# Kernel tuning notes

Hardware: AMD Instinct MI355X
Metric: run time of the kernel (lower is better)

## Reference

```python
import jax, jax.numpy as jnp
import numpy as np

MANTISA_BIT = 8.0  # mantisa_bit init arg


def conv3d(x, w, b, stride=1, pad=1):
    # x: [N,C,D,H,W], w: [O,I,kD,kH,kW]
    out = jax.lax.conv_general_dilated(
        x, w,
        window_strides=(stride, stride, stride),
        padding=[(pad, pad)] * 3,
        dimension_numbers=("NCDHW", "OIDHW", "NCDHW"),
    )
    return out + b.reshape(1, -1, 1, 1, 1)


def bfp_quant(x, ch_exp, m_bits):
    # Block floating point: shared per-channel exponent ch_exp [C],
    # signed mantissa with m_bits total bits. scale = 2^(m-1-exp);
    # q = clip(round(x*scale), -(2^(m-1)-1), 2^(m-1)-1)/scale
    scale = jnp.exp2(m_bits - 1.0 - ch_exp).reshape(1, -1, 1, 1, 1)
    lim = 2.0 ** (m_bits - 1.0) - 1.0
    return jnp.clip(jnp.round(x * scale), -lim, lim) / scale


def setup_inputs() -> dict:
    key = jax.random.key(0)
    ks = jax.random.split(key, 7)
    N, C_in, C_out, T, H, W, K = 8, 64, 64, 16, 56, 56, 3
    x = jax.random.normal(ks[0], (N, C_in, T, H, W), jnp.float32)
    w1 = jax.random.normal(ks[1], (C_out, C_in, K, K, K), jnp.float32) * 0.05
    b1 = jax.random.normal(ks[2], (C_out,), jnp.float32) * 0.05
    w2 = jax.random.normal(ks[3], (C_out, C_out, K, K, K), jnp.float32) * 0.05
    b2 = jax.random.normal(ks[4], (C_out,), jnp.float32) * 0.05
    # offline-optimized per-channel shared exponents (opt_exp_act_list[0], [1])
    exp1 = jax.random.randint(ks[5], (C_out,), 2, 6).astype(jnp.float32)
    exp2 = jax.random.randint(ks[6], (C_out,), 2, 6).astype(jnp.float32)
    return {"x": x, "w1": w1, "b1": b1, "w2": w2, "b2": b2,
            "exp1": exp1, "exp2": exp2}


def reference(x, w1, b1, w2, b2, exp1, exp2):
    # conv1 -> BFP quant -> ReLU
    res = conv3d(x, w1, b1)
    res = jax.nn.relu(bfp_quant(res, exp1, MANTISA_BIT))
    # conv2 -> BFP quant
    res = conv3d(res, w2, b2)
    res = bfp_quant(res, exp2, MANTISA_BIT)
    # identity shortcut (downsample=False) quantized with opt_exp_act_list[1]
    x_q = bfp_quant(x, exp2, MANTISA_BIT)
    return jax.nn.relu(x_q + res)
```

## Files before the change

kernel.cpp:

```cpp
#include <hip/hip_runtime.h>
#include <hip/hip_bf16.h>

#define Nn 8
#define Cc 64
#define Tt 16
#define Hh 56
#define Ww 56

typedef __bf16 bf16x8 __attribute__((ext_vector_type(8)));
typedef float f32x16 __attribute__((ext_vector_type(16)));
typedef unsigned short u16;
typedef unsigned int u32;

__device__ __forceinline__ u16 f32_to_bf16(float f) {
    u32 u = __float_as_uint(f);
    u32 r = (u + 0x7FFFu + ((u >> 16) & 1u)) >> 16;
    return (u16)r;
}
__device__ __forceinline__ float bf16_to_f32(u16 h) {
    return __uint_as_float(((u32)h) << 16);
}

__device__ __forceinline__ void gload16(const void* gsrc, void* lds) {
    __builtin_amdgcn_global_load_lds(
        (const __attribute__((address_space(1))) u32*)gsrc,
        (__attribute__((address_space(3))) u32*)lds, 16, 0, 0);
}

__global__ __launch_bounds__(256) void prep_w_kernel(
    const float* __restrict__ w1, const float* __restrict__ w2,
    u16* __restrict__ w1h, u16* __restrict__ w1l,
    u16* __restrict__ w2h, u16* __restrict__ w2l,
    u16* __restrict__ zpage)
{
    int idx = blockIdx.x * 256 + threadIdx.x;
    if (idx >= 221184) {
        ((uint4*)zpage)[idx - 221184] = make_uint4(0, 0, 0, 0);
        return;
    }
    int conv = idx / 110592;
    int rem  = idx % 110592;
    int tap  = rem >> 12;
    int co   = (rem >> 6) & 63;
    int ci   = rem & 63;
    const float* w = conv ? w2 : w1;
    float v = w[co * 1728 + ci * 27 + tap];
    u16 hi = f32_to_bf16(v);
    u16 lo = f32_to_bf16(v - bf16_to_f32(hi));
    int dst = tap * 4096 + co * 64 + ci;
    if (conv) { w2h[dst] = hi; w2l[dst] = lo; }
    else      { w1h[dst] = hi; w1l[dst] = lo; }
}

__global__ __launch_bounds__(256) void split_x_kernel(
    const float* __restrict__ x, u16* __restrict__ xh)
{
    __shared__ float tile[Cc][Hh + 1];
    const int tid = threadIdx.x;
    const int bid = blockIdx.x;
    const int h = bid % Hh;
    const int t = (bid / Hh) % Tt;
    const int n = bid / (Hh * Tt);
    for (int it = 0; it < 14; ++it) {
        int id = it * 256 + tid;
        int ci = id / Ww, w = id % Ww;
        tile[ci][w] = x[(((size_t)(n * Cc + ci) * Tt + t) * Hh + h) * Ww + w];
    }
    __syncthreads();
    const size_t obase = (size_t)bid * (Ww * Cc);
    for (int it = 0; it < 7; ++it) {
        int j = it * 256 + tid;
        int w = j >> 5, ci0 = (j & 31) << 1;
        u16 h0 = f32_to_bf16(tile[ci0][w]);
        u16 h1 = f32_to_bf16(tile[ci0 + 1][w]);
        *(ushort2*)(xh + obase + (size_t)w * Cc + ci0) = make_ushort2(h0, h1);
    }
}

#define SLICE_B 3712
#define A1_BUF  40960
#define B1_BUF  36864
#define C1_SMEM (2 * A1_BUF + 2 * B1_BUF)
#define C2_BOFF 40960
#define C2_SMEM 81920

__device__ __forceinline__ const bf16x8* frag_ptr(const char* base, int row, int slot) {
    int col = (slot * 16) ^ (((row >> 1) & 3) << 4);
    return (const bf16x8*)(base + row * 64 + col);
}

__global__ __launch_bounds__(512, 1) void conv1_mfma_kernel(
    const u16* __restrict__ xh,
    const u16* __restrict__ w1h, const u16* __restrict__ w1l,
    const float* __restrict__ b1, const float* __restrict__ e1,
    const u16* __restrict__ zpage, u16* __restrict__ res1)
{
    __shared__ __align__(16) char smem[C1_SMEM];

    const int tid = threadIdx.x;
    const int l = tid & 63, wid = tid >> 6;
    const int l31 = l & 31, hi5 = l >> 5;
    const int wbase = tid & ~63;
    const int bid = (blockIdx.x & 7) * 112 + (blockIdx.x >> 3);
    const int hb = bid % 7;
    const int t  = (bid / 7) % Tt;
    const int n  = bid / (7 * Tt);
    const int h0 = hb * 8;

    f32x16 acc[2][2] = {};

    auto ISSUE_A = [&](int slab, int abuf) {
        char* dst = smem + abuf * A1_BUF;
        const int cih = slab / 3, kd = slab % 3;
        const int td = t + kd - 1;
        const bool tdv = (td >= 0 && td < Tt);
        const size_t tdbase = (size_t)(n * Tt + (tdv ? td : 0)) * ((size_t)Hh * Ww * Cc);
#pragma unroll
        for (int it = 0; it < 5; ++it) {
            int fi = it * 512 + tid;
            int u = fi / 232, c = fi - u * 232;
            int r = c >> 2, slot = c & 3;
            int hh = h0 - 1 + u;
            int slog = slot ^ ((r >> 1) & 3);
            const u16* src = xh + tdbase
                + ((size_t)hh * Ww + (r - 1)) * Cc + cih * 32 + slog * 8;
            bool valid = tdv & (fi < 2320) & (hh >= 0) & (hh < Hh) & (r >= 1) & (r <= Ww);
            if (!valid) src = zpage;
            gload16(src, dst + (it * 512 + wbase) * 16);
        }
    };
    auto ISSUE_B = [&](int sub, int bbuf) {
        char* dst = smem + 2 * A1_BUF + bbuf * B1_BUF;
        const int slab = sub >> 1, hl = sub & 1;
        const int cih = slab / 3, kd = slab % 3;
        const u16* wsrc = hl ? w1l : w1h;
#pragma unroll
        for (int it = 0; it < 5; ++it) {
            int fi = it * 512 + tid;
            if (fi < 2304) {
                int u = fi >> 8, c = fi & 255;
                int co = c >> 2, slot = c & 3;
                int slog = slot ^ ((co >> 1) & 3);
                const u16* src = wsrc + (kd * 9 + u) * 4096 + co * 64 + cih * 32 + slog * 8;
                gload16(src, dst + (it * 512 + wbase) * 16);
            }
        }
    };

    ISSUE_A(0, 0);
    ISSUE_B(0, 0);
    asm volatile("s_waitcnt vmcnt(0)" ::: "memory");
    __builtin_amdgcn_s_barrier();
    __builtin_amdgcn_sched_barrier(0);

#pragma unroll 1
    for (int j = 0; j < 12; ++j) {
        if (j < 11) ISSUE_B(j + 1, (j + 1) & 1);
        if ((j & 1) && (j < 11)) ISSUE_A((j + 1) >> 1, ((j + 1) >> 1) & 1);
        __builtin_amdgcn_sched_barrier(0);
        const char* Acur = smem + (((j >> 1) & 1) * A1_BUF);
        const char* Bcur = smem + 2 * A1_BUF + ((j & 1) * B1_BUF);
        const char* Aw = Acur + (size_t)wid * SLICE_B;
#pragma unroll
        for (int kh = 0; kh < 3; ++kh) {
            const char* Ak = Aw + (size_t)kh * SLICE_B;
#pragma unroll
            for (int kw = 0; kw < 3; ++kw) {
                const int tap9 = kh * 3 + kw;
                bf16x8 a[2][2], b[2][2];
#pragma unroll
                for (int m = 0; m < 2; ++m)
#pragma unroll
                    for (int kk = 0; kk < 2; ++kk)
                        a[m][kk] = *frag_ptr(Ak, l31 + 32 * m + kw, kk * 2 + hi5);
#pragma unroll
                for (int nt = 0; nt < 2; ++nt)
#pragma unroll
                    for (int kk = 0; kk < 2; ++kk)
                        b[nt][kk] = *frag_ptr(Bcur + tap9 * 4096, l31 + 32 * nt, kk * 2 + hi5);
                __builtin_amdgcn_s_setprio(1);
#pragma unroll
                for (int m = 0; m < 2; ++m)
#pragma unroll
                    for (int nt = 0; nt < 2; ++nt)
#pragma unroll
                        for (int kk = 0; kk < 2; ++kk)
                            acc[m][nt] = __builtin_amdgcn_mfma_f32_32x32x16_bf16(
                                a[m][kk], b[nt][kk], acc[m][nt], 0, 0, 0);
                __builtin_amdgcn_s_setprio(0);
            }
        }
        __builtin_amdgcn_sched_barrier(0);
        __builtin_amdgcn_s_barrier();
        asm volatile("s_waitcnt vmcnt(0)" ::: "memory");
        __builtin_amdgcn_s_barrier();
        __builtin_amdgcn_sched_barrier(0);
    }

    const int h = h0 + wid;
    const size_t rowbase = ((size_t)(n * Tt + t) * Hh + h) * ((size_t)Ww * Cc);
#pragma unroll
    for (int nt = 0; nt < 2; ++nt) {
        int co = 32 * nt + l31;
        float e = e1[co];
        float sc = exp2f(7.0f - e), inv = exp2f(e - 7.0f);
        float bias = b1[co];
#pragma unroll
        for (int m = 0; m < 2; ++m)
#pragma unroll
            for (int reg = 0; reg < 16; ++reg) {
                int w = 32 * m + (reg & 3) + 8 * (reg >> 2) + 4 * hi5;
                if (w < Ww) {
                    float v = acc[m][nt][reg] + bias;
                    float q = rintf(v * sc);
                    q = fminf(fmaxf(q, -127.f), 127.f);
                    v = fmaxf(q * inv, 0.0f);
                    res1[rowbase + (size_t)w * Cc + co] = f32_to_bf16(v);
                }
            }
    }
}

__global__ __launch_bounds__(512, 2) void conv2_mfma_kernel(
    const u16* __restrict__ a, const u16* __restrict__ w2h,
    const float* __restrict__ b2, const float* __restrict__ e2,
    const float* __restrict__ x, const u16* __restrict__ zpage,
    float* __restrict__ out)
{
    __shared__ __align__(16) char smem[C2_SMEM];
    char* As = smem;
    char* Bs = smem + C2_BOFF;

    const int tid = threadIdx.x;
    const int l = tid & 63, wid = tid >> 6;
    const int l31 = l & 31, hi5 = l >> 5;
    const int wbase = tid & ~63;
    const int bid = (blockIdx.x & 7) * 112 + (blockIdx.x >> 3);
    const int hb = bid % 7;
    const int t  = (bid / 7) % Tt;
    const int n  = bid / (7 * Tt);
    const int h0 = hb * 8;

    f32x16 acc[2][2] = {};

#pragma unroll 1
    for (int cih = 0; cih < 2; ++cih) {
#pragma unroll 1
      for (int kd = 0; kd < 3; ++kd) {
        const int td = t + kd - 1;
        if (td < 0 || td >= Tt) continue;
        __builtin_amdgcn_sched_barrier(0);
        __builtin_amdgcn_s_barrier();
        __builtin_amdgcn_sched_barrier(0);
        {
          const size_t tdbase = (size_t)(n * Tt + td) * ((size_t)Hh * Ww * Cc);
#pragma unroll
          for (int it = 0; it < 5; ++it) {
            int fi = it * 512 + tid;
            int u = fi / 232, c = fi - u * 232;
            int r = c >> 2, slot = c & 3;
            int hh = h0 - 1 + u;
            int slog = slot ^ ((r >> 1) & 3);
            const u16* src = a + tdbase
                + ((size_t)hh * Ww + (r - 1)) * Cc + cih * 32 + slog * 8;
            bool valid = (fi < 2320) & (hh >= 0) & (hh < Hh) & (r >= 1) & (r <= Ww);
            if (!valid) src = zpage;
            gload16(src, As + (it * 512 + wbase) * 16);
          }
        }
        {
#pragma unroll
          for (int it = 0; it < 5; ++it) {
            int fi = it * 512 + tid;
            int u = fi >> 8, c = fi & 255;
            int co = c >> 2, slot = c & 3;
            int slog = slot ^ ((co >> 1) & 3);
            const u16* src = w2h + (kd * 9 + u) * 4096 + co * 64 + cih * 32 + slog * 8;
            if (fi >= 2304) src = zpage;
            gload16(src, Bs + (it * 512 + wbase) * 16);
          }
        }
        asm volatile("s_waitcnt vmcnt(0)" ::: "memory");
        __builtin_amdgcn_s_barrier();
        __builtin_amdgcn_sched_barrier(0);
        const char* Ab0 = As + (size_t)wid * SLICE_B;
#pragma unroll
        for (int kh = 0; kh < 3; ++kh) {
          const char* Ab = Ab0 + (size_t)kh * SLICE_B;
#pragma unroll
          for (int kw = 0; kw < 3; ++kw) {
            const int tap9 = kh * 3 + kw;
            bf16x8 a2[2][2], bh[2][2];
#pragma unroll
            for (int m = 0; m < 2; ++m)
#pragma unroll
              for (int kk = 0; kk < 2; ++kk)
                a2[m][kk] = *frag_ptr(Ab, l31 + 32 * m + kw, kk * 2 + hi5);
#pragma unroll
            for (int nt = 0; nt < 2; ++nt)
#pragma unroll
              for (int kk = 0; kk < 2; ++kk)
                bh[nt][kk] = *frag_ptr(Bs + tap9 * 4096, l31 + 32 * nt, kk * 2 + hi5);
            __builtin_amdgcn_s_setprio(1);
#pragma unroll
            for (int m = 0; m < 2; ++m)
#pragma unroll
              for (int nt = 0; nt < 2; ++nt)
#pragma unroll
                for (int kk = 0; kk < 2; ++kk)
                  acc[m][nt] = __builtin_amdgcn_mfma_f32_32x32x16_bf16(
                      a2[m][kk], bh[nt][kk], acc[m][nt], 0, 0, 0);
            __builtin_amdgcn_s_setprio(0);
          }
        }
      }
    }
    const int h = h0 + wid;
#pragma unroll
    for (int nt = 0; nt < 2; ++nt) {
      int co = 32 * nt + l31;
      float e = e2[co];
      float sc = exp2f(7.0f - e), inv = exp2f(e - 7.0f);
      float bias = b2[co];
#pragma unroll
      for (int m = 0; m < 2; ++m)
#pragma unroll
        for (int reg = 0; reg < 16; ++reg) {
          int w = 32 * m + (reg & 3) + 8 * (reg >> 2) + 4 * hi5;
          if (w < Ww) {
            float v = acc[m][nt][reg] + bias;
            float q = rintf(v * sc);
            q = fminf(fmaxf(q, -127.f), 127.f);
            v = q * inv;
            size_t xi = (((size_t)(n * Cc + co) * Tt + t) * Hh + h) * Ww + w;
            float xv = x[xi];
            float qx = rintf(xv * sc);
            qx = fminf(fmaxf(qx, -127.f), 127.f);
            out[xi] = fmaxf(qx * inv + v, 0.0f);
          }
        }
    }
}

extern "C" void kernel_launch(void* const* d_in, const int* in_sizes, int n_in,
                              void* d_out, int out_size, void* d_ws, size_t ws_size,
                              hipStream_t stream) {
    const float* x  = (const float*)d_in[0];
    const float* w1 = (const float*)d_in[1];
    const float* b1 = (const float*)d_in[2];
    const float* w2 = (const float*)d_in[3];
    const float* b2 = (const float*)d_in[4];
    const float* e1 = (const float*)d_in[5];
    const float* e2 = (const float*)d_in[6];

    u16* xh = (u16*)d_out;
    char* ws = (char*)d_ws;
    u16* w1h = (u16*)(ws);
    u16* w1l = (u16*)(ws + 221184);
    u16* w2h = (u16*)(ws + 442368);
    u16* w2l = (u16*)(ws + 663552);
    u16* zpage = (u16*)(ws + 884736);
    u16* res1  = (u16*)(ws + 888832);

    prep_w_kernel<<<865, 256, 0, stream>>>(w1, w2, w1h, w1l, w2h, w2l, zpage);
    split_x_kernel<<<Nn * Tt * Hh, 256, 0, stream>>>(x, xh);
    conv1_mfma_kernel<<<896, 512, 0, stream>>>(xh, w1h, w1l, b1, e1, zpage, res1);
    conv2_mfma_kernel<<<896, 512, 0, stream>>>(res1, w2h, b2, e2, x, zpage, (float*)d_out);
}
```

Measured before the change: 341.9 us.

## Halve block size so each wave computes two output rows, reusing B fragments

Both conv kernels now run 256 threads (4 waves) per block instead of 512, with each wave computing two h-rows and keeping doubled accumulators. The B (weight) fragments loaded from LDS are reused across both rows, which cuts LDS read traffic per MFMA. The global-to-LDS copy loops are rescaled to the smaller thread count. Accumulator registers double, and conv1 moves from one block per CU to a launch bound of two, so register pressure or spills are a risk. Conv2 is also left at two blocks with fewer waves, which may lower latency hiding.

```diff
diff --git a/kernel.cpp b/kernel.cpp
--- a/kernel.cpp
+++ b/kernel.cpp
@@ -89,7 +89,7 @@
     return (const bf16x8*)(base + row * 64 + col);
 }
 
-__global__ __launch_bounds__(512, 1) void conv1_mfma_kernel(
+__global__ __launch_bounds__(256, 2) void conv1_mfma_kernel(
     const u16* __restrict__ xh,
     const u16* __restrict__ w1h, const u16* __restrict__ w1l,
     const float* __restrict__ b1, const float* __restrict__ e1,
@@ -107,7 +107,7 @@
     const int n  = bid / (7 * Tt);
     const int h0 = hb * 8;
 
-    f32x16 acc[2][2] = {};
+    f32x16 acc[2][2][2] = {};
 
     auto ISSUE_A = [&](int slab, int abuf) {
         char* dst = smem + abuf * A1_BUF;
@@ -116,8 +116,8 @@
         const bool tdv = (td >= 0 && td < Tt);
         const size_t tdbase = (size_t)(n * Tt + (tdv ? td : 0)) * ((size_t)Hh * Ww * Cc);
 #pragma unroll
-        for (int it = 0; it < 5; ++it) {
-            int fi = it * 512 + tid;
+        for (int it = 0; it < 10; ++it) {
+            int fi = it * 256 + tid;
             int u = fi / 232, c = fi - u * 232;
             int r = c >> 2, slot = c & 3;
             int hh = h0 - 1 + u;
@@ -126,7 +126,7 @@
                 + ((size_t)hh * Ww + (r - 1)) * Cc + cih * 32 + slog * 8;
             bool valid = tdv & (fi < 2320) & (hh >= 0) & (hh < Hh) & (r >= 1) & (r <= Ww);
             if (!valid) src = zpage;
-            gload16(src, dst + (it * 512 + wbase) * 16);
+            gload16(src, dst + (it * 256 + wbase) * 16);
         }
     };
     auto ISSUE_B = [&](int sub, int bbuf) {
@@ -135,15 +135,13 @@
         const int cih = slab / 3, kd = slab % 3;
         const u16* wsrc = hl ? w1l : w1h;
 #pragma unroll
-        for (int it = 0; it < 5; ++it) {
-            int fi = it * 512 + tid;
-            if (fi < 2304) {
-                int u = fi >> 8, c = fi & 255;
-                int co = c >> 2, slot = c & 3;
-                int slog = slot ^ ((co >> 1) & 3);
-                const u16* src = wsrc + (kd * 9 + u) * 4096 + co * 64 + cih * 32 + slog * 8;
-                gload16(src, dst + (it * 512 + wbase) * 16);
-            }
+        for (int it = 0; it < 9; ++it) {
+            int fi = it * 256 + tid;
+            int u = fi >> 8, c = fi & 255;
+            int co = c >> 2, slot = c & 3;
+            int slog = slot ^ ((co >> 1) & 3);
+            const u16* src = wsrc + (kd * 9 + u) * 4096 + co * 64 + cih * 32 + slog * 8;
+            gload16(src, dst + (it * 256 + wbase) * 16);
         }
     };
 
@@ -160,34 +158,37 @@
         __builtin_amdgcn_sched_barrier(0);
         const char* Acur = smem + (((j >> 1) & 1) * A1_BUF);
         const char* Bcur = smem + 2 * A1_BUF + ((j & 1) * B1_BUF);
-        const char* Aw = Acur + (size_t)wid * SLICE_B;
 #pragma unroll
         for (int kh = 0; kh < 3; ++kh) {
-            const char* Ak = Aw + (size_t)kh * SLICE_B;
 #pragma unroll
             for (int kw = 0; kw < 3; ++kw) {
                 const int tap9 = kh * 3 + kw;
-                bf16x8 a[2][2], b[2][2];
-#pragma unroll
-                for (int m = 0; m < 2; ++m)
-#pragma unroll
-                    for (int kk = 0; kk < 2; ++kk)
-                        a[m][kk] = *frag_ptr(Ak, l31 + 32 * m + kw, kk * 2 + hi5);
+                bf16x8 b[2][2];
 #pragma unroll
                 for (int nt = 0; nt < 2; ++nt)
 #pragma unroll
                     for (int kk = 0; kk < 2; ++kk)
                         b[nt][kk] = *frag_ptr(Bcur + tap9 * 4096, l31 + 32 * nt, kk * 2 + hi5);
-                __builtin_amdgcn_s_setprio(1);
-#pragma unroll
-                for (int m = 0; m < 2; ++m)
-#pragma unroll
-                    for (int nt = 0; nt < 2; ++nt)
+#pragma unroll
+                for (int dh = 0; dh < 2; ++dh) {
+                    const char* Ak = Acur + (size_t)(2 * wid + dh + kh) * SLICE_B;
+                    bf16x8 a[2][2];
+#pragma unroll
+                    for (int m = 0; m < 2; ++m)
 #pragma unroll
                         for (int kk = 0; kk < 2; ++kk)
-                            acc[m][nt] = __builtin_amdgcn_mfma_f32_32x32x16_bf16(
-                                a[m][kk], b[nt][kk], acc[m][nt], 0, 0, 0);
-                __builtin_amdgcn_s_setprio(0);
+                            a[m][kk] = *frag_ptr(Ak, l31 + 32 * m + kw, kk * 2 + hi5);
+                    __builtin_amdgcn_s_setprio(1);
+#pragma unroll
+                    for (int m = 0; m < 2; ++m)
+#pragma unroll
+                        for (int nt = 0; nt < 2; ++nt)
+#pragma unroll
+                            for (int kk = 0; kk < 2; ++kk)
+                                acc[dh][m][nt] = __builtin_amdgcn_mfma_f32_32x32x16_bf16(
+                                    a[m][kk], b[nt][kk], acc[dh][m][nt], 0, 0, 0);
+                    __builtin_amdgcn_s_setprio(0);
+                }
             }
         }
         __builtin_amdgcn_sched_barrier(0);
@@ -197,31 +198,34 @@
         __builtin_amdgcn_sched_barrier(0);
     }
 
-    const int h = h0 + wid;
-    const size_t rowbase = ((size_t)(n * Tt + t) * Hh + h) * ((size_t)Ww * Cc);
-#pragma unroll
-    for (int nt = 0; nt < 2; ++nt) {
-        int co = 32 * nt + l31;
-        float e = e1[co];
-        float sc = exp2f(7.0f - e), inv = exp2f(e - 7.0f);
-        float bias = b1[co];
-#pragma unroll
-        for (int m = 0; m < 2; ++m)
-#pragma unroll
-            for (int reg = 0; reg < 16; ++reg) {
-                int w = 32 * m + (reg & 3) + 8 * (reg >> 2) + 4 * hi5;
-                if (w < Ww) {
-                    float v = acc[m][nt][reg] + bias;
-                    float q = rintf(v * sc);
-                    q = fminf(fmaxf(q, -127.f), 127.f);
-                    v = fmaxf(q * inv, 0.0f);
-                    res1[rowbase + (size_t)w * Cc + co] = f32_to_bf16(v);
+#pragma unroll
+    for (int dh = 0; dh < 2; ++dh) {
+        const int h = h0 + 2 * wid + dh;
+        const size_t rowbase = ((size_t)(n * Tt + t) * Hh + h) * ((size_t)Ww * Cc);
+#pragma unroll
+        for (int nt = 0; nt < 2; ++nt) {
+            int co = 32 * nt + l31;
+            float e = e1[co];
+            float sc = exp2f(7.0f - e), inv = exp2f(e - 7.0f);
+            float bias = b1[co];
+#pragma unroll
+            for (int m = 0; m < 2; ++m)
+#pragma unroll
+                for (int reg = 0; reg < 16; ++reg) {
+                    int w = 32 * m + (reg & 3) + 8 * (reg >> 2) + 4 * hi5;
+                    if (w < Ww) {
+                        float v = acc[dh][m][nt][reg] + bias;
+                        float q = rintf(v * sc);
+                        q = fminf(fmaxf(q, -127.f), 127.f);
+                        v = fmaxf(q * inv, 0.0f);
+                        res1[rowbase + (size_t)w * Cc + co] = f32_to_bf16(v);
+                    }
                 }
-            }
-    }
-}
-
-__global__ __launch_bounds__(512, 2) void conv2_mfma_kernel(
+        }
+    }
+}
+
+__global__ __launch_bounds__(256, 2) void conv2_mfma_kernel(
     const u16* __restrict__ a, const u16* __restrict__ w2h,
     const float* __restrict__ b2, const float* __restrict__ e2,
     const float* __restrict__ x, const u16* __restrict__ zpage,
@@ -241,7 +245,7 @@
     const int n  = bid / (7 * Tt);
     const int h0 = hb * 8;
 
-    f32x16 acc[2][2] = {};
+    f32x16 acc[2][2][2] = {};
 
 #pragma unroll 1
     for (int cih = 0; cih < 2; ++cih) {
@@ -255,8 +259,8 @@
         {
           const size_t tdbase = (size_t)(n * Tt + td) * ((size_t)Hh * Ww * Cc);
 #pragma unroll
-          for (int it = 0; it < 5; ++it) {
-            int fi = it * 512 + tid;
+          for (int it = 0; it < 10; ++it) {
+            int fi = it * 256 + tid;
             int u = fi / 232, c = fi - u * 232;
             int r = c >> 2, slot = c & 3;
             int hh = h0 - 1 + u;
@@ -265,80 +269,85 @@
                 + ((size_t)hh * Ww + (r - 1)) * Cc + cih * 32 + slog * 8;
             bool valid = (fi < 2320) & (hh >= 0) & (hh < Hh) & (r >= 1) & (r <= Ww);
             if (!valid) src = zpage;
-            gload16(src, As + (it * 512 + wbase) * 16);
+            gload16(src, As + (it * 256 + wbase) * 16);
           }
         }
         {
 #pragma unroll
-          for (int it = 0; it < 5; ++it) {
-            int fi = it * 512 + tid;
+          for (int it = 0; it < 9; ++it) {
+            int fi = it * 256 + tid;
             int u = fi >> 8, c = fi & 255;
             int co = c >> 2, slot = c & 3;
             int slog = slot ^ ((co >> 1) & 3);
             const u16* src = w2h + (kd * 9 + u) * 4096 + co * 64 + cih * 32 + slog * 8;
-            if (fi >= 2304) src = zpage;
-            gload16(src, Bs + (it * 512 + wbase) * 16);
+            gload16(src, Bs + (it * 256 + wbase) * 16);
           }
         }
         asm volatile("s_waitcnt vmcnt(0)" ::: "memory");
         __builtin_amdgcn_s_barrier();
         __builtin_amdgcn_sched_barrier(0);
-        const char* Ab0 = As + (size_t)wid * SLICE_B;
 #pragma unroll
         for (int kh = 0; kh < 3; ++kh) {
-          const char* Ab = Ab0 + (size_t)kh * SLICE_B;
 #pragma unroll
           for (int kw = 0; kw < 3; ++kw) {
             const int tap9 = kh * 3 + kw;
-            bf16x8 a2[2][2], bh[2][2];
-#pragma unroll
-            for (int m = 0; m < 2; ++m)
+            bf16x8 b[2][2];
+#pragma unroll
+            for (int nt = 0; nt < 2; ++nt)
 #pragma unroll
               for (int kk = 0; kk < 2; ++kk)
-                a2[m][kk] = *frag_ptr(Ab, l31 + 32 * m + kw, kk * 2 + hi5);
-#pragma unroll
-            for (int nt = 0; nt < 2; ++nt)
-#pragma unroll
-              for (int kk = 0; kk < 2; ++kk)
-                bh[nt][kk] = *frag_ptr(Bs + tap9 * 4096, l31 + 32 * nt, kk * 2 + hi5);
-            __builtin_amdgcn_s_setprio(1);
-#pragma unroll
-            for (int m = 0; m < 2; ++m)
-#pragma unroll
-              for (int nt = 0; nt < 2; ++nt)
+                b[nt][kk] = *frag_ptr(Bs + tap9 * 4096, l31 + 32 * nt, kk * 2 + hi5);
+#pragma unroll
+            for (int dh = 0; dh < 2; ++dh) {
+              const char* Ak = As + (size_t)(2 * wid + dh + kh) * SLICE_B;
+              bf16x8 a2[2][2];
+#pragma unroll
+              for (int m = 0; m < 2; ++m)
 #pragma unroll
                 for (int kk = 0; kk < 2; ++kk)
-                  acc[m][nt] = __builtin_amdgcn_mfma_f32_32x32x16_bf16(
-                      a2[m][kk], bh[nt][kk], acc[m][nt], 0, 0, 0);
-            __builtin_amdgcn_s_setprio(0);
+                  a2[m][kk] = *frag_ptr(Ak, l31 + 32 * m + kw, kk * 2 + hi5);
+              __builtin_amdgcn_s_setprio(1);
+#pragma unroll
+              for (int m = 0; m < 2; ++m)
+#pragma unroll
+                for (int nt = 0; nt < 2; ++nt)
+#pragma unroll
+                  for (int kk = 0; kk < 2; ++kk)
+                    acc[dh][m][nt] = __builtin_amdgcn_mfma_f32_32x32x16_bf16(
+                        a2[m][kk], b[nt][kk], acc[dh][m][nt], 0, 0, 0);
+              __builtin_amdgcn_s_setprio(0);
+            }
           }
         }
       }
     }
-    const int h = h0 + wid;
-#pragma unroll
-    for (int nt = 0; nt < 2; ++nt) {
-      int co = 32 * nt + l31;
-      float e = e2[co];
-      float sc = exp2f(7.0f - e), inv = exp2f(e - 7.0f);
-      float bias = b2[co];
-#pragma unroll
-      for (int m = 0; m < 2; ++m)
-#pragma unroll
-        for (int reg = 0; reg < 16; ++reg) {
-          int w = 32 * m + (reg & 3) + 8 * (reg >> 2) + 4 * hi5;
-          if (w < Ww) {
-            float v = acc[m][nt][reg] + bias;
-            float q = rintf(v * sc);
-            q = fminf(fmaxf(q, -127.f), 127.f);
-            v = q * inv;
-            size_t xi = (((size_t)(n * Cc + co) * Tt + t) * Hh + h) * Ww + w;
-            float xv = x[xi];
-            float qx = rintf(xv * sc);
-            qx = fminf(fmaxf(qx, -127.f), 127.f);
-            out[xi] = fmaxf(qx * inv + v, 0.0f);
+#pragma unroll
+    for (int dh = 0; dh < 2; ++dh) {
+      const int h = h0 + 2 * wid + dh;
+#pragma unroll
+      for (int nt = 0; nt < 2; ++nt) {
+        int co = 32 * nt + l31;
+        float e = e2[co];
+        float sc = exp2f(7.0f - e), inv = exp2f(e - 7.0f);
+        float bias = b2[co];
+#pragma unroll
+        for (int m = 0; m < 2; ++m)
+#pragma unroll
+          for (int reg = 0; reg < 16; ++reg) {
+            int w = 32 * m + (reg & 3) + 8 * (reg >> 2) + 4 * hi5;
+            if (w < Ww) {
+              float v = acc[dh][m][nt][reg] + bias;
+              float q = rintf(v * sc);
+              q = fminf(fmaxf(q, -127.f), 127.f);
+              v = q * inv;
+              size_t xi = (((size_t)(n * Cc + co) * Tt + t) * Hh + h) * Ww + w;
+              float xv = x[xi];
+              float qx = rintf(xv * sc);
+              qx = fminf(fmaxf(qx, -127.f), 127.f);
+              out[xi] = fmaxf(qx * inv + v, 0.0f);
+            }
           }
-        }
+      }
     }
 }
 
@@ -364,6 +373,6 @@
 
     prep_w_kernel<<<865, 256, 0, stream>>>(w1, w2, w1h, w1l, w2h, w2l, zpage);
     split_x_kernel<<<Nn * Tt * Hh, 256, 0, stream>>>(x, xh);
-    conv1_mfma_kernel<<<896, 512, 0, stream>>>(xh, w1h, w1l, b1, e1, zpage, res1);
-    conv2_mfma_kernel<<<896, 512, 0, stream>>>(res1, w2h, b2, e2, x, zpage, (float*)d_out);
-}
+    conv1_mfma_kernel<<<896, 256, 0, stream>>>(xh, w1h, w1l, b1, e1, zpage, res1);
+    conv2_mfma_kernel<<<896, 256, 0, stream>>>(res1, w2h, b2, e2, x, zpage, (float*)d_out);
+}
```

New measurement: 363.0 us. 6.2% more time.
